# Performance work log

Measured on AMD Instinct MI355X. Metric: run time of the kernel, lower is better.

The kernel has to match this reference:

```python
import jax, jax.numpy as jnp
import numpy as np

V = 50257  # vocab_size
H = 512    # d_model
S = 512    # source length
B = 8      # batch
T = 64     # decode steps


def setup_inputs() -> dict:
    key = jax.random.key(0)
    k1, k2, k3, k4, k5, k6 = jax.random.split(key, 6)
    src_full = jax.random.randint(k1, (S, B), 0, V, dtype=jnp.int32)
    decode_output = jax.random.normal(k2, (T, B, H), dtype=jnp.float32)
    decode_attn = jax.random.uniform(k3, (B, T, S), dtype=jnp.float32)
    memory = jax.random.normal(k4, (S, B, H), dtype=jnp.float32)
    # learned params: gen_proj (H->V) and prob_proj (H->1)
    W_gen = jax.random.normal(k5, (H, V), dtype=jnp.float32) / np.sqrt(H)
    b_gen = jnp.zeros((V,), dtype=jnp.float32)
    W_prob = jax.random.normal(k6, (H, 1), dtype=jnp.float32) / np.sqrt(H)
    b_prob = jnp.zeros((1,), dtype=jnp.float32)
    return {
        "src_full": src_full,
        "decode_output": decode_output,
        "decode_attn": decode_attn,
        "memory": memory,
        "W_gen": W_gen,
        "b_gen": b_gen,
        "W_prob": W_prob,
        "b_prob": b_prob,
    }


def reference(src_full, decode_output, decode_attn, memory, W_gen, b_gen, W_prob, b_prob):
    # context[t,b,h] = sum_s attn[b,t,s] * memory[s,b,h]
    context = jnp.einsum("bts,sbh->tbh", decode_attn, memory)  # [T,B,H]
    prob = jax.nn.sigmoid(context @ W_prob + b_prob)           # [T,B,1] copy gate p_gen
    gen_logits = prob * jax.nn.softmax(decode_output @ W_gen + b_gen, axis=-1)  # [T,B,V]

    # scatter-add attention mass onto vocab slots: copy[t,b, src_full[s,b]] += attn[b,t,s]
    attn_tbs = jnp.transpose(decode_attn, (1, 0, 2))  # [T,B,S]
    idx = src_full.T                                  # [B,S]
    ti = jnp.arange(T)[:, None, None]
    bi = jnp.arange(B)[None, :, None]
    copy_logits = jnp.zeros((T, B, V), dtype=decode_attn.dtype).at[ti, bi, idx[None, :, :]].add(attn_tbs)
    copy_logits = (1.0 - prob) * jax.nn.softmax(copy_logits, axis=-1)

    return jnp.log(gen_logits + copy_logits)
```

## Files before the change

### kernel.cpp

```cpp
#include <hip/hip_runtime.h>
#include <hip/hip_bf16.h>
#include <math.h>

#define VV 50257
#define VP 50304
#define HH 512
#define SS 512
#define BB 8
#define TT 64
#define MM (TT*BB)

typedef __bf16 bf16x2 __attribute__((ext_vector_type(2)));
typedef __bf16 bf16x4 __attribute__((ext_vector_type(4)));
typedef __bf16 bf16x8 __attribute__((ext_vector_type(8)));
typedef float  f32x4  __attribute__((ext_vector_type(4)));
typedef float f4u __attribute__((vector_size(16), aligned(4)));

__device__ __forceinline__ __bf16 f2b(float f) {
    unsigned u = __builtin_bit_cast(unsigned, f);
    unsigned r = (u + 0x7fffu + ((u >> 16) & 1u)) >> 16;
    unsigned short s = (unsigned short)r;
    return __builtin_bit_cast(__bf16, s);
}

__device__ __forceinline__ void gl2lds16(const void* g, void* l) {
    __builtin_amdgcn_global_load_lds(
        (const __attribute__((address_space(1))) unsigned*)g,
        (__attribute__((address_space(3))) unsigned*)l, 16, 0, 0);
}

#define WAITV(n) asm volatile("s_waitcnt vmcnt(" #n ")" ::: "memory")

#define NW8 3200
__global__ __launch_bounds__(256) void k_pre(const float* __restrict__ W,
                                             __bf16* __restrict__ Wt8,
                                             const float* __restrict__ A,
                                             __bf16* __restrict__ Ab,
                                             const float* __restrict__ mem,
                                             const float* __restrict__ Wp,
                                             float* __restrict__ mw) {
    int tid = threadIdx.x;
    int bx = blockIdx.x;
    if (bx < NW8) {
        int cx = bx % 50, kb = bx / 50;
        int nb = cx * 1024 + tid * 4;
        if (nb >= VP) return;
        const float* Wr = W + (size_t)(kb * 8) * VV + nb;
        float v[8][4];
        if (nb + 4 <= VV) {
#pragma unroll
            for (int r = 0; r < 8; r++) {
                f4u x = *(const f4u*)(Wr + (size_t)r * VV);
#pragma unroll
                for (int j = 0; j < 4; j++) v[r][j] = x[j];
            }
        } else {
#pragma unroll
            for (int r = 0; r < 8; r++)
#pragma unroll
                for (int j = 0; j < 4; j++)
                    v[r][j] = (nb + j < VV) ? Wr[(size_t)r * VV + j] : 0.f;
        }
#pragma unroll
        for (int j = 0; j < 4; j++) {
            bf16x8 o = {f2b(v[0][j]), f2b(v[1][j]), f2b(v[2][j]), f2b(v[3][j]),
                        f2b(v[4][j]), f2b(v[5][j]), f2b(v[6][j]), f2b(v[7][j])};
            *(bf16x8*)&Wt8[((size_t)kb * VP + nb + j) * 8] = o;
        }
    } else if (bx < NW8 + 256) {
        int i = ((bx - NW8) * 256 + tid) * 4;
        float4 va = *(const float4*)&A[i];
        bf16x4 o = {f2b(va.x), f2b(va.y), f2b(va.z), f2b(va.w)};
        *(bf16x4*)&Ab[i] = o;
    } else {
        int bxm = bx - (NW8 + 256);
        int row = bxm * 4 + (tid >> 6);
        int lane = tid & 63;
        const float* mp = mem + (size_t)row * HH;
        float acc = 0.f;
#pragma unroll
        for (int i = 0; i < HH / 64; i++)
            acc += mp[lane + 64 * i] * Wp[lane + 64 * i];
#pragma unroll
        for (int off = 32; off > 0; off >>= 1) acc += __shfl_down(acc, off);
        if (lane == 0) mw[row] = acc;
    }
}

template<bool BF16OUT>
__global__ __launch_bounds__(512, 4) void k_gemm7(const __bf16* __restrict__ Ab,
                                                  const __bf16* __restrict__ Wt8,
                                                  const float* __restrict__ bias,
                                                  float* __restrict__ Cf,
                                                  __bf16* __restrict__ Cb,
                                                  float* __restrict__ Zrow) {
    __shared__ __bf16 As[3][8192];
    __shared__ __bf16 Bs[3][4096];
    __shared__ float zred[256];

    const int tid  = threadIdx.x;
    const int lane = tid & 63;
    const int wave = tid >> 6;
    const int l15  = lane & 15;
    const int quad = lane >> 4;
    const int wr = (wave >> 1) * 64;
    const int wc = (wave & 1) * 64;

    int L = blockIdx.x + gridDim.x * blockIdx.y;
    int xcd = L & 7, i8 = L >> 3;
    int nid = (xcd < 2 ? xcd * 99 : 2 * 99 + (xcd - 2) * 98) + i8;
    const int row0 = (nid & 1) * 256;
    const int col0 = (nid >> 1) * 128;

    size_t offA[2];
#pragma unroll
    for (int q = 0; q < 2; q++)
        offA[q] = (size_t)(row0 + (2 * wave + q) * 16 + l15) * HH + quad * 8;
    const size_t offB = (size_t)quad * VP * 8 +
                        (size_t)(col0 + wave * 16 + l15) * 8;

#define STAGE(buf, k0)                                                       \
    do {                                                                     \
        gl2lds16(Ab + offA[0] + (k0), &As[buf][(2 * wave) * 512]);           \
        gl2lds16(Ab + offA[1] + (k0), &As[buf][(2 * wave + 1) * 512]);       \
        gl2lds16(Wt8 + offB + (size_t)(k0) * VP, &Bs[buf][wave * 512]);      \
    } while (0)

    f32x4 acc[4][4] = {};

    STAGE(0, 0);
    STAGE(1, 32);
#pragma unroll
    for (int it = 0; it < 16; ++it) {
        if (it < 15) WAITV(3);
        else         WAITV(0);
        __builtin_amdgcn_s_barrier();
        if (it < 14) STAGE((it + 2) % 3, (it + 2) * 32);
        const __bf16* Al = &As[it % 3][0];
        const __bf16* Bl = &Bs[it % 3][0];
        bf16x8 af[4], bfv[4];
#pragma unroll
        for (int mt = 0; mt < 4; mt++)
            af[mt] = *(const bf16x8*)&Al[((wr >> 4) + mt) * 512 + lane * 8];
#pragma unroll
        for (int nt = 0; nt < 4; nt++)
            bfv[nt] = *(const bf16x8*)&Bl[((wc >> 4) + nt) * 512 + lane * 8];
        __builtin_amdgcn_s_setprio(1);
#pragma unroll
        for (int mt = 0; mt < 4; mt++)
#pragma unroll
            for (int nt = 0; nt < 4; nt++)
                acc[mt][nt] = __builtin_amdgcn_mfma_f32_16x16x32_bf16(
                    af[mt], bfv[nt], acc[mt][nt], 0, 0, 0);
        __builtin_amdgcn_s_setprio(0);
    }
#undef STAGE

    __syncthreads();
    if (tid < 256) zred[tid] = 0.f;
    __syncthreads();

#pragma unroll
    for (int mt = 0; mt < 4; mt++) {
        float esum[4] = {0.f, 0.f, 0.f, 0.f};
#pragma unroll
        for (int nt = 0; nt < 4; nt++) {
            int c = col0 + wc + nt * 16 + l15;
            if (c < VV) {
                float bv = bias[c];
#pragma unroll
                for (int i = 0; i < 4; i++) {
                    int r = row0 + wr + mt * 16 + quad * 4 + i;
                    float l = acc[mt][nt][i] + bv;
                    if (BF16OUT) Cb[(size_t)r * VP + c] = f2b(l);
                    else         Cf[(size_t)r * VV + c] = l;
                    esum[i] += __expf(l);
                }
            }
        }
#pragma unroll
        for (int i = 0; i < 4; i++) {
            float e = esum[i];
            e += __shfl_xor(e, 1);
            e += __shfl_xor(e, 2);
            e += __shfl_xor(e, 4);
            e += __shfl_xor(e, 8);
            if (l15 == 0)
                atomicAdd(&zred[wr + mt * 16 + quad * 4 + i], e);
        }
    }
    __syncthreads();
    if (tid < 256) atomicAdd(&Zrow[row0 + tid], zred[tid]);
}

#define HT 1024
#define NBW 1572

__device__ __forceinline__ void build_hash(const int* __restrict__ src,
                                           const float* __restrict__ ap,
                                           int b, int tid,
                                           int* keys, float* vals, unsigned* bmap,
                                           float* red, int* s_D, float* s_Zc) {
    for (int i = tid; i < HT; i += 256) { keys[i] = -1; vals[i] = 0.f; }
    for (int i = tid; i < NBW; i += 256) bmap[i] = 0u;
    if (tid == 0) *s_D = 0;
    __syncthreads();

    for (int s = tid; s < SS; s += 256) {
        int idx = src[s * BB + b];
        float v = ap[s];
        unsigned h = ((unsigned)idx * 2654435761u) >> 22;
        while (true) {
            int old = atomicCAS(&keys[h], -1, idx);
            if (old == -1 || old == idx) { atomicAdd(&vals[h], v); break; }
            h = (h + 1) & (HT - 1);
        }
    }
    __syncthreads();

    float lsum = 0.f; int dloc = 0;
    for (int i = tid; i < HT; i += 256) {
        int k = keys[i];
        if (k != -1) {
            lsum += __expf(vals[i]); dloc++;
            atomicOr(&bmap[(unsigned)k >> 5], 1u << (k & 31));
        }
    }
    atomicAdd(s_D, dloc);
    red[tid] = lsum; __syncthreads();
    for (int st = 128; st > 0; st >>= 1) {
        if (tid < st) red[tid] += red[tid + st];
        __syncthreads();
    }
    if (tid == 0) *s_Zc = (float)(VV - *s_D) + red[0];
    __syncthreads();
}

#define HV (VP / 2)
__global__ __launch_bounds__(1024) void k_final2(const int* __restrict__ src,
                                                 const float* __restrict__ attn,
                                                 const float* __restrict__ mw,
                                                 const float* __restrict__ bp,
                                                 const float* __restrict__ Zrow,
                                                 const __bf16* __restrict__ LG,
                                                 float* __restrict__ out) {
    __shared__ int      keys[HT];
    __shared__ float    vals[HT];
    __shared__ unsigned bmap[NBW];
    __shared__ float    red[1024];
    __shared__ float    red2[1024];
    __shared__ int      s_D;
    __shared__ float    s_Zc;
    __shared__ float    s_p;

    int r = blockIdx.y;
    int half = blockIdx.x;
    int t = r / BB, b = r % BB;
    int tid = threadIdx.x;
    const float* ap = attn + ((size_t)b * TT + t) * SS;

    { keys[tid] = -1; vals[tid] = 0.f; }
    for (int i = tid; i < NBW; i += 1024) bmap[i] = 0u;
    if (tid == 0) s_D = 0;
    __syncthreads();

    float pv = 0.f;
    if (tid < SS) {
        int idx = src[tid * BB + b];
        float av = ap[tid];
        pv = av * mw[tid * BB + b];
        unsigned h = ((unsigned)idx * 2654435761u) >> 22;
        while (true) {
            int old = atomicCAS(&keys[h], -1, idx);
            if (old == -1 || old == idx) { atomicAdd(&vals[h], av); break; }
            h = (h + 1) & (HT - 1);
        }
    }
    __syncthreads();

    float lsum = 0.f;
    {
        int k = keys[tid];
        bool occ = (k != -1);
        if (occ) {
            lsum = __expf(vals[tid]);
            atomicOr(&bmap[(unsigned)k >> 5], 1u << (k & 31));
        }
        unsigned long long m = __ballot(occ);
        if ((tid & 63) == 0) atomicAdd(&s_D, __popcll(m));
    }
    red[tid] = lsum; red2[tid] = pv; __syncthreads();
    for (int st = 512; st > 0; st >>= 1) {
        if (tid < st) { red[tid] += red[tid + st]; red2[tid] += red2[tid + st]; }
        __syncthreads();
    }
    if (tid == 0) {
        s_Zc = (float)(VV - s_D) + red[0];
        s_p  = 1.f / (1.f + expf(-(red2[0] + bp[0])));
    }
    __syncthreads();

    float p = s_p;
    float pinvZ = p / Zrow[r];
    float qinvZc = (1.f - p) / s_Zc;

    const __bf16* lrow = LG + (size_t)r * VP;
    float* orow = out + (size_t)r * VV;

    int base = half * HV;
    for (int v0 = base + tid * 8; v0 < base + HV; v0 += 8192) {
        bf16x8 l8 = *(const bf16x8*)&lrow[v0];
        unsigned bits = (bmap[v0 >> 5] >> (v0 & 31)) & 0xFFu;
        if (bits == 0u && v0 + 8 <= VV) {
#pragma unroll
            for (int e = 0; e < 8; e++)
                orow[v0 + e] = __logf(pinvZ * __expf((float)l8[e]) + qinvZc);
        } else {
#pragma unroll
            for (int e = 0; e < 8; e++) {
                int v = v0 + e;
                if (v < VV) {
                    float l = (float)l8[e];
                    float c = 1.f;
                    if ((bits >> e) & 1u) {
                        unsigned h = ((unsigned)v * 2654435761u) >> 22;
                        while (true) {
                            int k = keys[h];
                            if (k == v) { c = __expf(vals[h]); break; }
                            if (k == -1) break;
                            h = (h + 1) & (HT - 1);
                        }
                    }
                    orow[v] = __logf(pinvZ * __expf(l) + qinvZc * c);
                }
            }
        }
    }
}

#define CHUNKS 6283
__global__ __launch_bounds__(256) void k_final_s(const int* __restrict__ src,
                                                 const float* __restrict__ attn,
                                                 const float* __restrict__ mw,
                                                 const float* __restrict__ bp,
                                                 const float* __restrict__ Zrow,
                                                 float* __restrict__ out) {
    __shared__ int      keys[HT];
    __shared__ float    vals[HT];
    __shared__ unsigned bmap[NBW];
    __shared__ float    red[256];
    __shared__ int      s_D;
    __shared__ float    s_Zc;
    __shared__ float    s_p;

    int r = blockIdx.y;
    int t = r / BB, b = r % BB;
    int tid = threadIdx.x;
    const float* ap = attn + ((size_t)b * TT + t) * SS;

    float pacc = ap[tid] * mw[tid * BB + b] +
                 ap[tid + 256] * mw[(tid + 256) * BB + b];
    red[tid] = pacc; __syncthreads();
    for (int st = 128; st > 0; st >>= 1) {
        if (tid < st) red[tid] += red[tid + st];
        __syncthreads();
    }
    if (tid == 0) s_p = 1.f / (1.f + expf(-(red[0] + bp[0])));
    __syncthreads();

    build_hash(src, ap, b, tid, keys, vals, bmap, red, &s_D, &s_Zc);

    float p = s_p;
    float pinvZ = p / Zrow[r];
    float qinvZc = (1.f - p) / s_Zc;

    int c0 = blockIdx.x * CHUNKS;
    int c1 = c0 + CHUNKS; if (c1 > VV) c1 = VV;
    float* rowp = out + (size_t)r * VV;

    for (int v = c0 + tid; v < c1; v += 256) {
        float l = rowp[v];
        float c = 1.f;
        if ((bmap[v >> 5] >> (v & 31)) & 1u) {
            unsigned h = ((unsigned)v * 2654435761u) >> 22;
            while (true) {
                int k = keys[h];
                if (k == v) { c = __expf(vals[h]); break; }
                if (k == -1) break;
                h = (h + 1) & (HT - 1);
            }
        }
        rowp[v] = __logf(pinvZ * __expf(l) + qinvZc * c);
    }
}

extern "C" void kernel_launch(void* const* d_in, const int* in_sizes, int n_in,
                              void* d_out, int out_size, void* d_ws, size_t ws_size,
                              hipStream_t stream) {
    const int*   src_full      = (const int*)d_in[0];
    const float* decode_output = (const float*)d_in[1];
    const float* decode_attn   = (const float*)d_in[2];
    const float* memory        = (const float*)d_in[3];
    const float* W_gen         = (const float*)d_in[4];
    const float* b_gen         = (const float*)d_in[5];
    const float* W_prob        = (const float*)d_in[6];
    const float* b_prob        = (const float*)d_in[7];
    float* out = (float*)d_out;

    float* ws   = (float*)d_ws;
    float* mw   = ws;
    float* Z    = ws + 4608;
    __bf16* Ab  = (__bf16*)(ws + 5120);
    __bf16* Wt8 = (__bf16*)(ws + 5120 + 131072);
    __bf16* LG  = Wt8 + (size_t)VP * HH;

    size_t base_b = (size_t)(5120 + 131072) * sizeof(float);
    size_t wt_b   = (size_t)VP * HH * 2;
    size_t lg_b   = (size_t)MM * VP * 2;
    bool full = ws_size >= base_b + wt_b + lg_b;

    k_pre<<<NW8 + 256 + 1024, 256, 0, stream>>>(
        W_gen, Wt8, decode_output, Ab, memory, W_prob, mw);
    hipMemsetAsync(Z, 0, MM * sizeof(float), stream);

    dim3 ggrid(MM / 256, VP / 128);
    if (full) {
        k_gemm7<true><<<ggrid, 512, 0, stream>>>(Ab, Wt8, b_gen, nullptr, LG, Z);
        dim3 fgrid(2, MM);
        k_final2<<<fgrid, 1024, 0, stream>>>(src_full, decode_attn, mw, b_prob,
                                             Z, LG, out);
    } else {
        k_gemm7<false><<<ggrid, 512, 0, stream>>>(Ab, Wt8, b_gen, out, nullptr, Z);
        dim3 fgrid((VV + CHUNKS - 1) / CHUNKS, MM);
        k_final_s<<<fgrid, 256, 0, stream>>>(src_full, decode_attn, mw, b_prob,
                                             Z, out);
    }
}
```

Before: 311.5 us.

## Widen GEMM blocks to 16 waves with 4-stage pipeline, drop memset, single-block final rows

The GEMM kernel now launches 1024 threads per block, with 16 waves each computing a 64x32 sub-tile instead of 8 waves with 64x64. The LDS pipeline deepens from 3 to 4 stages, and the wait counts are adjusted per wave group. The aim is more latency hiding and more waves in flight. The Z-row memset is folded into the preprocessing kernel as an extra block, removing one API call. The final kernel now uses one 1024-thread block per row instead of two half-row blocks, which avoids rebuilding the hash table twice. The risks are higher register and LDS pressure, which may lower occupancy, and less parallelism in the final pass.

```diff
diff --git a/kernel.cpp b/kernel.cpp
--- a/kernel.cpp
+++ b/kernel.cpp
@@ -38,7 +38,8 @@
                                              __bf16* __restrict__ Ab,
                                              const float* __restrict__ mem,
                                              const float* __restrict__ Wp,
-                                             float* __restrict__ mw) {
+                                             float* __restrict__ mw,
+                                             float* __restrict__ Z) {
     int tid = threadIdx.x;
     int bx = blockIdx.x;
     if (bx < NW8) {
@@ -72,7 +73,7 @@
         float4 va = *(const float4*)&A[i];
         bf16x4 o = {f2b(va.x), f2b(va.y), f2b(va.z), f2b(va.w)};
         *(bf16x4*)&Ab[i] = o;
-    } else {
+    } else if (bx < NW8 + 256 + 1024) {
         int bxm = bx - (NW8 + 256);
         int row = bxm * 4 + (tid >> 6);
         int lane = tid & 63;
@@ -84,18 +85,21 @@
 #pragma unroll
         for (int off = 32; off > 0; off >>= 1) acc += __shfl_down(acc, off);
         if (lane == 0) mw[row] = acc;
+    } else {
+        Z[tid] = 0.f;
+        Z[tid + 256] = 0.f;
     }
 }
 
 template<bool BF16OUT>
-__global__ __launch_bounds__(512, 4) void k_gemm7(const __bf16* __restrict__ Ab,
-                                                  const __bf16* __restrict__ Wt8,
-                                                  const float* __restrict__ bias,
-                                                  float* __restrict__ Cf,
-                                                  __bf16* __restrict__ Cb,
-                                                  float* __restrict__ Zrow) {
-    __shared__ __bf16 As[3][8192];
-    __shared__ __bf16 Bs[3][4096];
+__global__ __launch_bounds__(1024, 4) void k_gemm8(const __bf16* __restrict__ Ab,
+                                                   const __bf16* __restrict__ Wt8,
+                                                   const float* __restrict__ bias,
+                                                   float* __restrict__ Cf,
+                                                   __bf16* __restrict__ Cb,
+                                                   float* __restrict__ Zrow) {
+    __shared__ __bf16 As[4][8192];
+    __shared__ __bf16 Bs[4][4096];
     __shared__ float zred[256];
 
     const int tid  = threadIdx.x;
@@ -103,8 +107,8 @@
     const int wave = tid >> 6;
     const int l15  = lane & 15;
     const int quad = lane >> 4;
-    const int wr = (wave >> 1) * 64;
-    const int wc = (wave & 1) * 64;
+    const int wr = (wave >> 2) * 64;
+    const int wc = (wave & 3) * 32;
 
     int L = blockIdx.x + gridDim.x * blockIdx.y;
     int xcd = L & 7, i8 = L >> 3;
@@ -112,44 +116,49 @@
     const int row0 = (nid & 1) * 256;
     const int col0 = (nid >> 1) * 128;
 
-    size_t offA[2];
-#pragma unroll
-    for (int q = 0; q < 2; q++)
-        offA[q] = (size_t)(row0 + (2 * wave + q) * 16 + l15) * HH + quad * 8;
+    const size_t offA = (size_t)(row0 + wave * 16 + l15) * HH + quad * 8;
     const size_t offB = (size_t)quad * VP * 8 +
-                        (size_t)(col0 + wave * 16 + l15) * 8;
-
-#define STAGE(buf, k0)                                                       \
-    do {                                                                     \
-        gl2lds16(Ab + offA[0] + (k0), &As[buf][(2 * wave) * 512]);           \
-        gl2lds16(Ab + offA[1] + (k0), &As[buf][(2 * wave + 1) * 512]);       \
-        gl2lds16(Wt8 + offB + (size_t)(k0) * VP, &Bs[buf][wave * 512]);      \
+                        (size_t)(col0 + (wave & 7) * 16 + l15) * 8;
+
+#define STAGE(buf, k0)                                                      \
+    do {                                                                    \
+        gl2lds16(Ab + offA + (k0), &As[buf][wave * 512]);                   \
+        if (wave < 8)                                                       \
+            gl2lds16(Wt8 + offB + (size_t)(k0) * VP, &Bs[buf][wave * 512]); \
     } while (0)
 
-    f32x4 acc[4][4] = {};
+    f32x4 acc[4][2] = {};
 
     STAGE(0, 0);
     STAGE(1, 32);
+    STAGE(2, 64);
 #pragma unroll
     for (int it = 0; it < 16; ++it) {
-        if (it < 15) WAITV(3);
-        else         WAITV(0);
+        if (wave < 8) {
+            if (it <= 13)      WAITV(4);
+            else if (it == 14) WAITV(2);
+            else               WAITV(0);
+        } else {
+            if (it <= 13)      WAITV(2);
+            else if (it == 14) WAITV(1);
+            else               WAITV(0);
+        }
         __builtin_amdgcn_s_barrier();
-        if (it < 14) STAGE((it + 2) % 3, (it + 2) * 32);
-        const __bf16* Al = &As[it % 3][0];
-        const __bf16* Bl = &Bs[it % 3][0];
-        bf16x8 af[4], bfv[4];
+        if (it <= 12) STAGE((it + 3) & 3, (it + 3) * 32);
+        const __bf16* Al = &As[it & 3][0];
+        const __bf16* Bl = &Bs[it & 3][0];
+        bf16x8 af[4], bfv[2];
 #pragma unroll
         for (int mt = 0; mt < 4; mt++)
             af[mt] = *(const bf16x8*)&Al[((wr >> 4) + mt) * 512 + lane * 8];
 #pragma unroll
-        for (int nt = 0; nt < 4; nt++)
+        for (int nt = 0; nt < 2; nt++)
             bfv[nt] = *(const bf16x8*)&Bl[((wc >> 4) + nt) * 512 + lane * 8];
         __builtin_amdgcn_s_setprio(1);
 #pragma unroll
         for (int mt = 0; mt < 4; mt++)
 #pragma unroll
-            for (int nt = 0; nt < 4; nt++)
+            for (int nt = 0; nt < 2; nt++)
                 acc[mt][nt] = __builtin_amdgcn_mfma_f32_16x16x32_bf16(
                     af[mt], bfv[nt], acc[mt][nt], 0, 0, 0);
         __builtin_amdgcn_s_setprio(0);
@@ -164,7 +173,7 @@
     for (int mt = 0; mt < 4; mt++) {
         float esum[4] = {0.f, 0.f, 0.f, 0.f};
 #pragma unroll
-        for (int nt = 0; nt < 4; nt++) {
+        for (int nt = 0; nt < 2; nt++) {
             int c = col0 + wc + nt * 16 + l15;
             if (c < VV) {
                 float bv = bias[c];
@@ -236,8 +245,7 @@
     __syncthreads();
 }
 
-#define HV (VP / 2)
-__global__ __launch_bounds__(1024) void k_final2(const int* __restrict__ src,
+__global__ __launch_bounds__(1024) void k_final3(const int* __restrict__ src,
                                                  const float* __restrict__ attn,
                                                  const float* __restrict__ mw,
                                                  const float* __restrict__ bp,
@@ -253,8 +261,7 @@
     __shared__ float    s_Zc;
     __shared__ float    s_p;
 
-    int r = blockIdx.y;
-    int half = blockIdx.x;
+    int r = blockIdx.x;
     int t = r / BB, b = r % BB;
     int tid = threadIdx.x;
     const float* ap = attn + ((size_t)b * TT + t) * SS;
@@ -307,8 +314,7 @@
     const __bf16* lrow = LG + (size_t)r * VP;
     float* orow = out + (size_t)r * VV;
 
-    int base = half * HV;
-    for (int v0 = base + tid * 8; v0 < base + HV; v0 += 8192) {
+    for (int v0 = tid * 8; v0 < VP; v0 += 8192) {
         bf16x8 l8 = *(const bf16x8*)&lrow[v0];
         unsigned bits = (bmap[v0 >> 5] >> (v0 & 31)) & 0xFFu;
         if (bits == 0u && v0 + 8 <= VV) {
@@ -419,18 +425,16 @@
     size_t lg_b   = (size_t)MM * VP * 2;
     bool full = ws_size >= base_b + wt_b + lg_b;
 
-    k_pre<<<NW8 + 256 + 1024, 256, 0, stream>>>(
-        W_gen, Wt8, decode_output, Ab, memory, W_prob, mw);
-    hipMemsetAsync(Z, 0, MM * sizeof(float), stream);
+    k_pre<<<NW8 + 256 + 1024 + 1, 256, 0, stream>>>(
+        W_gen, Wt8, decode_output, Ab, memory, W_prob, mw, Z);
 
     dim3 ggrid(MM / 256, VP / 128);
     if (full) {
-        k_gemm7<true><<<ggrid, 512, 0, stream>>>(Ab, Wt8, b_gen, nullptr, LG, Z);
-        dim3 fgrid(2, MM);
-        k_final2<<<fgrid, 1024, 0, stream>>>(src_full, decode_attn, mw, b_prob,
-                                             Z, LG, out);
+        k_gemm8<true><<<ggrid, 1024, 0, stream>>>(Ab, Wt8, b_gen, nullptr, LG, Z);
+        k_final3<<<MM, 1024, 0, stream>>>(src_full, decode_attn, mw, b_prob,
+                                          Z, LG, out);
     } else {
-        k_gemm7<false><<<ggrid, 512, 0, stream>>>(Ab, Wt8, b_gen, out, nullptr, Z);
+        k_gemm8<false><<<ggrid, 1024, 0, stream>>>(Ab, Wt8, b_gen, out, nullptr, Z);
         dim3 fgrid((VV + CHUNKS - 1) / CHUNKS, MM);
         k_final_s<<<fgrid, 256, 0, stream>>>(src_full, decode_attn, mw, b_prob,
                                              Z, out);
```

Measured after the change: 324.0 us. 4.0% more time.
